# Optimization experiments

Measured on AMD Instinct MI355X. Metric: run time of the kernel, lower is better.

## Reference

```python
import jax, jax.numpy as jnp
import numpy as np

SCALE = 0.02

def setup_inputs() -> dict:
    key = jax.random.key(0)
    k1, k2 = jax.random.split(key)
    B, D, T, H = 2, 1024, 2048, 16
    x = jax.random.normal(k1, (B, D, T), dtype=jnp.float32)
    qkv = jax.random.normal(k2, (3, H, D, D // H), dtype=jnp.float32) * SCALE
    return {"x": x, "qkv": qkv}

def reference(x, qkv):
    B, D, T = x.shape
    H = qkv.shape[1]
    # fused QKV projection: (B,D,T) x (3,H,D,Dh) -> (3,B,H,T,Dh)
    proj = jnp.einsum('bdt,nhdD->nbhtD', x, qkv)
    q, k, v = proj[0], proj[1], proj[2]
    scale = jnp.sqrt(jnp.asarray(D // H, dtype=x.dtype))
    # scores: (B,H,T,T)
    attn = jax.nn.softmax(jnp.einsum('bhtD,bhTD->bhtT', q, k) / scale, axis=-1)
    # weighted values, head dim placed before time: (B,H,Dh,T)
    out = jnp.einsum('bhtT,bhTD->bhDt', attn, v)
    return out.reshape(B, D, T)
```

## Files before the change

kernel.cpp:

```cpp
#include <hip/hip_runtime.h>

#define B_ 2
#define D_ 1024
#define T_ 2048
#define H_ 16
#define DH_ 64
#define BH_ (B_ * H_)

typedef __attribute__((ext_vector_type(8))) short bf16x8;
typedef __attribute__((ext_vector_type(8))) unsigned short u16x8;
typedef __attribute__((ext_vector_type(4))) float f32x4;

__device__ __forceinline__ unsigned cvt_pk_bf16(float a, float b) {
    unsigned r;
    asm("v_cvt_pk_bf16_f32 %0, %1, %2" : "=v"(r) : "v"(a), "v"(b));
    return r;
}

__device__ __forceinline__ void gload_lds16(const unsigned short* g, unsigned short* l) {
    __builtin_amdgcn_global_load_lds(
        (const __attribute__((address_space(1))) unsigned int*)(const void*)g,
        (__attribute__((address_space(3))) unsigned int*)(void*)l,
        16, 0, 0);
}

__global__ __launch_bounds__(256) void xpose_kernel(
    const float* __restrict__ x, unsigned short* __restrict__ xT)
{
    __shared__ __align__(16) unsigned short Ls[64][68];
    const int t0 = blockIdx.x * 64;
    const int d0 = blockIdx.y * 64;
    const int b  = blockIdx.z;
    const int tid = threadIdx.x;

    const float* xb = x + (size_t)b * D_ * T_ + (size_t)d0 * T_ + t0;
    #pragma unroll
    for (int p = 0; p < 4; p++) {
        int i4  = tid + p * 256;
        int row = i4 >> 4;
        int c4  = (i4 & 15) << 2;
        float4 v = *(const float4*)(xb + (size_t)row * T_ + c4);
        uint2 u;
        u.x = cvt_pk_bf16(v.x, v.y);
        u.y = cvt_pk_bf16(v.z, v.w);
        *(uint2*)&Ls[row][c4] = u;
    }
    __syncthreads();
    unsigned short* ob = xT + (size_t)b * T_ * D_ + (size_t)t0 * D_ + d0;
    #pragma unroll
    for (int p = 0; p < 2; p++) {
        int i    = tid + p * 256;
        int orow = i >> 3;
        int oc8  = (i & 7) * 8;
        u16x8 tv;
        #pragma unroll
        for (int j = 0; j < 8; j++) tv[j] = Ls[oc8 + j][orow];
        *(u16x8*)(ob + (size_t)orow * D_ + oc8) = tv;
    }
}

__global__ __launch_bounds__(256) void wpose_kernel(
    const float* __restrict__ w, unsigned short* __restrict__ wT)
{
    __shared__ __align__(16) unsigned short Ls[64][68];
    const int d0 = blockIdx.x * 64;
    const int nh = blockIdx.y;
    const int tid = threadIdx.x;

    const float* wb = w + (size_t)nh * D_ * DH_ + (size_t)d0 * DH_;
    #pragma unroll
    for (int p = 0; p < 4; p++) {
        int i4  = tid + p * 256;
        int row = i4 >> 4;
        int c4  = (i4 & 15) << 2;
        float4 v = *(const float4*)(wb + (size_t)row * DH_ + c4);
        uint2 u;
        u.x = cvt_pk_bf16(v.x, v.y);
        u.y = cvt_pk_bf16(v.z, v.w);
        *(uint2*)&Ls[row][c4] = u;
    }
    __syncthreads();
    unsigned short* ob = wT + (size_t)nh * DH_ * D_ + d0;
    #pragma unroll
    for (int p = 0; p < 2; p++) {
        int i    = tid + p * 256;
        int orow = i >> 3;
        int oc8  = (i & 7) * 8;
        u16x8 tv;
        #pragma unroll
        for (int j = 0; j < 8; j++) tv[j] = Ls[oc8 + j][orow];
        *(u16x8*)(ob + (size_t)orow * D_ + oc8) = tv;
    }
}

__global__ __launch_bounds__(256, 2) void proj_mfma_kernel(
    const unsigned short* __restrict__ xT, const unsigned short* __restrict__ wT,
    unsigned short* __restrict__ qk, unsigned short* __restrict__ vT)
{
    __shared__ __align__(16) unsigned short Buf[32768];
    unsigned short* Es = Buf;

    const int t0 = blockIdx.x * 128;
    const int y  = blockIdx.y;
    const int n  = y >> 4;
    const int b  = (y >> 3) & 1;
    const int hp = y & 7;

    const unsigned short* xb = xT + (size_t)b * T_ * D_ + (size_t)t0 * D_;
    const unsigned short* wb = wT + (size_t)(n * 16 + 2 * hp) * DH_ * D_;

    const int tid  = threadIdx.x;
    const int wv   = tid >> 6;
    const int lane = tid & 63;
    const int c15  = lane & 15;
    const int quad = lane >> 4;
    const int tq   = (wv & 1) * 64;
    const int dq   = (wv >> 1) * 64;

    const int srow8 = lane >> 3;
    const int sch8  = (lane & 7) * 8;

    f32x4 acc[4][4];
    #pragma unroll
    for (int mt = 0; mt < 4; mt++)
        #pragma unroll
        for (int nt = 0; nt < 4; nt++)
            acc[mt][nt] = (f32x4){0.f, 0.f, 0.f, 0.f};

    auto stage = [&](int k0, int bsel) {
        unsigned short* Xs = Buf + bsel * 16384;
        unsigned short* Ws = Xs + 8192;
        #pragma unroll
        for (int i = 0; i < 4; i++) {
            int row = wv * 32 + i * 8;
            gload_lds16(xb + (size_t)(row + srow8) * D_ + k0 + sch8,
                        Xs + row * 64);
            gload_lds16(wb + (size_t)(row + srow8) * D_ + k0 + sch8,
                        Ws + row * 64);
        }
    };

    stage(0, 0);
    int ks = 0;
    for (int k0 = 0; k0 < D_; k0 += 64, ks ^= 1) {
        __syncthreads();

        if (k0 + 64 < D_) stage(k0 + 64, ks ^ 1);

        unsigned short* Xs = Buf + ks * 16384;
        unsigned short* Ws = Xs + 8192;

        bf16x8 af[4][2], bf[4][2];
        #pragma unroll
        for (int mt = 0; mt < 4; mt++)
            #pragma unroll
            for (int s = 0; s < 2; s++)
                af[mt][s] = *(bf16x8*)&Xs[(tq + mt * 16 + c15) * 64 + quad * 8 + s * 32];
        #pragma unroll
        for (int nt = 0; nt < 4; nt++)
            #pragma unroll
            for (int s = 0; s < 2; s++)
                bf[nt][s] = *(bf16x8*)&Ws[(dq + nt * 16 + c15) * 64 + quad * 8 + s * 32];

        #pragma unroll
        for (int mt = 0; mt < 4; mt++)
            #pragma unroll
            for (int nt = 0; nt < 4; nt++)
                #pragma unroll
                for (int s = 0; s < 2; s++)
                    acc[mt][nt] = __builtin_amdgcn_mfma_f32_16x16x32_bf16(
                        af[mt][s], bf[nt][s], acc[mt][nt], 0, 0, 0);
    }

    const float scale = (n == 0) ? 0.125f * 1.44269504f : 1.0f;
    __syncthreads();
    #pragma unroll
    for (int mt = 0; mt < 4; mt++)
        #pragma unroll
        for (int nt = 0; nt < 4; nt++)
            #pragma unroll
            for (int r = 0; r < 4; r++) {
                float v = acc[mt][nt][r] * scale;
                Es[(tq + mt * 16 + quad * 4 + r) * 136 + dq + nt * 16 + c15] =
                    (unsigned short)cvt_pk_bf16(v, v);
            }
    __syncthreads();

    if (n < 2) {
        #pragma unroll
        for (int p = 0; p < 8; p++) {
            int i    = tid + p * 256;
            int row  = i >> 4;
            int col8 = (i & 15) * 8;
            int head = col8 >> 6;
            unsigned short* ob = qk +
                ((size_t)(n * 32 + b * 16 + 2 * hp + head) * T_ + t0 + row) * DH_ + (col8 & 63);
            *(u16x8*)ob = *(u16x8*)&Es[row * 136 + col8];
        }
    } else {
        #pragma unroll
        for (int p = 0; p < 8; p++) {
            int i    = tid + p * 256;
            int orow = i >> 4;
            int oc8  = (i & 15) * 8;
            int head = orow >> 6;
            u16x8 tv;
            #pragma unroll
            for (int j = 0; j < 8; j++) tv[j] = Es[(oc8 + j) * 136 + orow];
            unsigned short* ob = vT +
                (size_t)(b * 16 + 2 * hp + head) * DH_ * T_ +
                (size_t)(orow & 63) * T_ + t0 + oc8;
            *(u16x8*)ob = tv;
        }
    }
}

__global__ __launch_bounds__(256, 4) void attn_mfma_kernel(
    const unsigned short* __restrict__ qk, const unsigned short* __restrict__ vT,
    float* __restrict__ out)
{
    __shared__ __align__(16) unsigned short Sm[20480];

    const int flat = blockIdx.x;
    const int bh   = (flat & 7) * 4 + ((flat >> 3) >> 5);
    const int t0   = ((flat >> 3) & 31) * 64;

    const unsigned short* qg = qk + ((size_t)bh * T_ + t0) * DH_;
    const unsigned short* kg = qk + ((size_t)(BH_ + bh) * T_) * DH_;
    const unsigned short* vg = vT + (size_t)bh * DH_ * T_;

    const int tid  = threadIdx.x;
    const int wv   = tid >> 6;
    const int lane = tid & 63;
    const int c15  = lane & 15;
    const int quad = lane >> 4;
    const int swz  = (c15 & 7) * 8;
    const int h7   = c15 & 7;

    unsigned short* Ps = Sm + 16384 + wv * 1024;

    const int srow = tid >> 3;
    const int sch  = tid & 7;
    const int ssw  = ((sch ^ (srow & 7)) * 8);

    bf16x8 bq[2];
    #pragma unroll
    for (int s = 0; s < 2; s++)
        bq[s] = *(const bf16x8*)(qg + (size_t)(wv * 16 + c15) * DH_ + quad * 8 + s * 32);

    float lsum = 0.f;
    f32x4 Oacc[4];
    #pragma unroll
    for (int nt = 0; nt < 4; nt++) Oacc[nt] = (f32x4){0.f, 0.f, 0.f, 0.f};

    u16x8 kreg[2], vreg[2];
    #pragma unroll
    for (int p = 0; p < 2; p++) {
        int row = srow + p * 32;
        kreg[p] = *(const u16x8*)(kg + (size_t)row * DH_ + sch * 8);
        vreg[p] = *(const u16x8*)(vg + (size_t)row * T_ + sch * 8);
    }
    #pragma unroll
    for (int p = 0; p < 2; p++) {
        int row = srow + p * 32;
        *(u16x8*)&Sm[row * 64 + ssw]        = kreg[p];
        *(u16x8*)&Sm[4096 + row * 64 + ssw] = vreg[p];
    }

    for (int tau = 0; tau < T_; tau += 64) {
        const int cur = (tau >> 6) & 1;
        unsigned short* Ks = Sm + cur * 8192;
        unsigned short* Vs = Ks + 4096;
        __syncthreads();

        const bool pf = (tau + 64 < T_);
        if (pf) {
            #pragma unroll
            for (int p = 0; p < 2; p++) {
                int row = srow + p * 32;
                kreg[p] = *(const u16x8*)(kg + (size_t)(tau + 64 + row) * DH_ + sch * 8);
                vreg[p] = *(const u16x8*)(vg + (size_t)row * T_ + tau + 64 + sch * 8);
            }
        }

        #pragma unroll
        for (int mt = 0; mt < 4; mt++) {
            f32x4 sa = (f32x4){0.f, 0.f, 0.f, 0.f};
            #pragma unroll
            for (int s = 0; s < 2; s++) {
                bf16x8 ak = *(bf16x8*)&Ks[(mt * 16 + c15) * 64 +
                                          (((quad + 4 * s) ^ h7) * 8)];
                sa = __builtin_amdgcn_mfma_f32_16x16x32_bf16(ak, bq[s], sa, 0, 0, 0);
            }
            float p0 = __builtin_amdgcn_exp2f(sa[0]);
            float p1 = __builtin_amdgcn_exp2f(sa[1]);
            float p2 = __builtin_amdgcn_exp2f(sa[2]);
            float p3 = __builtin_amdgcn_exp2f(sa[3]);
            lsum += (p0 + p1) + (p2 + p3);
            uint2 pk;
            pk.x = cvt_pk_bf16(p0, p1);
            pk.y = cvt_pk_bf16(p2, p3);
            *(uint2*)&Ps[c15 * 64 + ((mt * 16 + quad * 4) ^ swz)] = pk;
        }

        #pragma unroll
        for (int s = 0; s < 2; s++) {
            bf16x8 ap = *(bf16x8*)&Ps[c15 * 64 + ((quad * 8 + s * 32) ^ swz)];
            #pragma unroll
            for (int nt = 0; nt < 4; nt++) {
                bf16x8 bv = *(bf16x8*)&Vs[(nt * 16 + c15) * 64 +
                                          (((quad + 4 * s) ^ h7) * 8)];
                Oacc[nt] = __builtin_amdgcn_mfma_f32_16x16x32_bf16(ap, bv, Oacc[nt], 0, 0, 0);
            }
        }

        if (pf) {
            unsigned short* Kn = Sm + (1 - cur) * 8192;
            #pragma unroll
            for (int p = 0; p < 2; p++) {
                int row = srow + p * 32;
                *(u16x8*)&Kn[row * 64 + ssw]        = kreg[p];
                *(u16x8*)&Kn[4096 + row * 64 + ssw] = vreg[p];
            }
        }
    }

    lsum += __shfl_xor(lsum, 16);
    lsum += __shfl_xor(lsum, 32);
    float linv[4];
    #pragma unroll
    for (int r = 0; r < 4; r++)
        linv[r] = 1.0f / __shfl(lsum, quad * 4 + r);

    __syncthreads();
    float* Osw = (float*)(void*)Sm + wv * 1088;
    #pragma unroll
    for (int nt = 0; nt < 4; nt++)
        #pragma unroll
        for (int r = 0; r < 4; r++)
            Osw[(nt * 16 + c15) * 17 + quad * 4 + r] = Oacc[nt][r] * linv[r];

    const int b = bh >> 4, h = bh & 15;
    float* og = out + (size_t)b * D_ * T_ + (size_t)(h * DH_) * T_ + t0 + wv * 16;
    #pragma unroll
    for (int p = 0; p < 4; p++) {
        int idx = lane + p * 64;
        int dh  = idx >> 2;
        int qs  = (idx & 3) * 4;
        float4 v = *(float4*)&Osw[dh * 17 + qs];
        *(float4*)(og + (size_t)dh * T_ + qs) = v;
    }
}

extern "C" void kernel_launch(void* const* d_in, const int* in_sizes, int n_in,
                              void* d_out, int out_size, void* d_ws, size_t ws_size,
                              hipStream_t stream)
{
    const float* x = (const float*)d_in[0];
    const float* w = (const float*)d_in[1];
    float* out = (float*)d_out;

    unsigned short* qk = (unsigned short*)d_ws;
    unsigned short* vT = (unsigned short*)((char*)d_ws + (24u << 20));
    unsigned short* xT = (unsigned short*)((char*)d_ws + (32u << 20));
    unsigned short* wT = (unsigned short*)((char*)d_ws + (40u << 20));

    xpose_kernel<<<dim3(T_ / 64, D_ / 64, B_), 256, 0, stream>>>(x, xT);
    wpose_kernel<<<dim3(D_ / 64, 3 * H_), 256, 0, stream>>>(w, wT);
    proj_mfma_kernel<<<dim3(T_ / 128, 48), 256, 0, stream>>>(xT, wT, qk, vT);
    attn_mfma_kernel<<<1024, 256, 0, stream>>>(qk, vT, out);
}
```

Before: 168.0 us.

## Swizzle projection LDS tiles, single-buffer staging, raise occupancy to three blocks

The projection GEMM now XOR-swizzles the 16-byte chunk index when staging X and W tiles into LDS and applies the same swizzle when reading MFMA fragments, to avoid LDS bank conflicts. The double-buffered prefetch is replaced by a single buffer with load-then-sync per k step, which shrinks shared memory so launch bounds can request three blocks per CU. The trade is that global-to-LDS loads no longer overlap with MFMA compute within a block, relying on more resident blocks to hide latency.

```diff
diff --git a/kernel.cpp b/kernel.cpp
--- a/kernel.cpp
+++ b/kernel.cpp
@@ -93,11 +93,13 @@
     }
 }
 
-__global__ __launch_bounds__(256, 2) void proj_mfma_kernel(
+__global__ __launch_bounds__(256, 3) void proj_mfma_kernel(
     const unsigned short* __restrict__ xT, const unsigned short* __restrict__ wT,
     unsigned short* __restrict__ qk, unsigned short* __restrict__ vT)
 {
-    __shared__ __align__(16) unsigned short Buf[32768];
+    __shared__ __align__(16) unsigned short Buf[17408];
+    unsigned short* Xs = Buf;
+    unsigned short* Ws = Buf + 8192;
     unsigned short* Es = Buf;
 
     const int t0 = blockIdx.x * 128;
@@ -118,7 +120,8 @@
     const int dq   = (wv >> 1) * 64;
 
     const int srow8 = lane >> 3;
-    const int sch8  = (lane & 7) * 8;
+    const int ssw   = ((lane & 7) ^ srow8) * 8;
+    const int h7c   = c15 & 7;
 
     f32x4 acc[4][4];
     #pragma unroll
@@ -127,40 +130,29 @@
         for (int nt = 0; nt < 4; nt++)
             acc[mt][nt] = (f32x4){0.f, 0.f, 0.f, 0.f};
 
-    auto stage = [&](int k0, int bsel) {
-        unsigned short* Xs = Buf + bsel * 16384;
-        unsigned short* Ws = Xs + 8192;
+    for (int k0 = 0; k0 < D_; k0 += 64) {
+        __syncthreads();
         #pragma unroll
         for (int i = 0; i < 4; i++) {
-            int row = wv * 32 + i * 8;
-            gload_lds16(xb + (size_t)(row + srow8) * D_ + k0 + sch8,
-                        Xs + row * 64);
-            gload_lds16(wb + (size_t)(row + srow8) * D_ + k0 + sch8,
-                        Ws + row * 64);
-        }
-    };
-
-    stage(0, 0);
-    int ks = 0;
-    for (int k0 = 0; k0 < D_; k0 += 64, ks ^= 1) {
+            int row0 = wv * 32 + i * 8;
+            gload_lds16(xb + (size_t)(row0 + srow8) * D_ + k0 + ssw, Xs + row0 * 64);
+            gload_lds16(wb + (size_t)(row0 + srow8) * D_ + k0 + ssw, Ws + row0 * 64);
+        }
         __syncthreads();
 
-        if (k0 + 64 < D_) stage(k0 + 64, ks ^ 1);
-
-        unsigned short* Xs = Buf + ks * 16384;
-        unsigned short* Ws = Xs + 8192;
-
         bf16x8 af[4][2], bf[4][2];
         #pragma unroll
         for (int mt = 0; mt < 4; mt++)
             #pragma unroll
             for (int s = 0; s < 2; s++)
-                af[mt][s] = *(bf16x8*)&Xs[(tq + mt * 16 + c15) * 64 + quad * 8 + s * 32];
+                af[mt][s] = *(bf16x8*)&Xs[(tq + mt * 16 + c15) * 64 +
+                                          (((quad + 4 * s) ^ h7c) * 8)];
         #pragma unroll
         for (int nt = 0; nt < 4; nt++)
             #pragma unroll
             for (int s = 0; s < 2; s++)
-                bf[nt][s] = *(bf16x8*)&Ws[(dq + nt * 16 + c15) * 64 + quad * 8 + s * 32];
+                bf[nt][s] = *(bf16x8*)&Ws[(dq + nt * 16 + c15) * 64 +
+                                          (((quad + 4 * s) ^ h7c) * 8)];
 
         #pragma unroll
         for (int mt = 0; mt < 4; mt++)
```

After: 169.4 us. About the same (+0.8%).
